# Kernel tuning notes

Measured on AMD Instinct MI355X. Metric: run time of the kernel, lower is better.

Reference implementation:

```python
import jax, jax.numpy as jnp
import numpy as np

N_NODES = 50000
N_EDGES = 1600000
N_GRAPHS = 1000


def setup_inputs() -> dict:
    key = jax.random.key(0)
    ks = jax.random.split(key, 16)
    s = 0.1
    return {
        "x": jax.random.normal(ks[0], (N_NODES, 7), jnp.float32),
        "edge_attr": jax.random.normal(ks[1], (N_EDGES, 4), jnp.float32),
        "edge_index": jax.random.randint(ks[2], (2, N_EDGES), 0, N_NODES),
        "batch": jnp.sort(jax.random.randint(ks[3], (N_NODES,), 0, N_GRAPHS)),
        "We1": jax.random.normal(ks[4], (4, 7), jnp.float32) * s,
        "be1": jnp.zeros((7,), jnp.float32),
        "W1a": jax.random.normal(ks[5], (7, 64), jnp.float32) * s,
        "b1a": jnp.zeros((64,), jnp.float32),
        "W1b": jax.random.normal(ks[6], (64, 64), jnp.float32) * s,
        "b1b": jnp.zeros((64,), jnp.float32),
        "We2": jax.random.normal(ks[7], (4, 64), jnp.float32) * s,
        "be2": jnp.zeros((64,), jnp.float32),
        "W2a": jax.random.normal(ks[8], (64, 64), jnp.float32) * s,
        "b2a": jnp.zeros((64,), jnp.float32),
        "W2b": jax.random.normal(ks[9], (64, 64), jnp.float32) * s,
        "b2b": jnp.zeros((64,), jnp.float32),
        "Wfc": jax.random.normal(ks[10], (64, 12), jnp.float32) * s,
        "bfc": jnp.zeros((12,), jnp.float32),
    }


def _gine_conv(h, edge_attr, src, dst, We, be, Wa, ba, Wb, bb, n_nodes):
    # GINEConv (eps=0): out = nn(h + sum_j relu(h[src] + lin(edge_attr)))
    e = edge_attr @ We + be                      # [E, d]
    msg = jax.nn.relu(h[src] + e)                # [E, d] gather + add + relu
    aggr = jax.ops.segment_sum(msg, dst, num_segments=n_nodes)  # scatter-sum
    z = h + aggr
    return jax.nn.relu(z @ Wa + ba) @ Wb + bb


def reference(x, edge_attr, edge_index, batch,
              We1, be1, W1a, b1a, W1b, b1b,
              We2, be2, W2a, b2a, W2b, b2b,
              Wfc, bfc):
    src, dst = edge_index[0], edge_index[1]
    n = x.shape[0]
    h = jax.nn.relu(_gine_conv(x, edge_attr, src, dst, We1, be1, W1a, b1a, W1b, b1b, n))
    h = jax.nn.relu(_gine_conv(h, edge_attr, src, dst, We2, be2, W2a, b2a, W2b, b2b, n))
    # global mean pool over batch index
    sums = jax.ops.segment_sum(h, batch, num_segments=N_GRAPHS)          # [G, 64]
    cnt = jax.ops.segment_sum(jnp.ones((n,), h.dtype), batch, num_segments=N_GRAPHS)
    pooled = sums / jnp.maximum(cnt, 1.0)[:, None]
    return pooled @ Wfc + bfc                                            # [G, 12]
```

## Files before the change

### kernel.cpp

```cpp
#include <hip/hip_runtime.h>

typedef unsigned char uchar;
typedef unsigned short ushort;
typedef unsigned int uint;

constexpr int NN = 50000;
constexpr int NE = 1600000;
constexpr int NG = 1000;
constexpr int NB2 = 196;
constexpr int TILE = 4096;
constexpr int NTILE = (NE + TILE - 1) / TILE;
constexpr int SPAN_CAP = 9216;
constexpr int MSTRIDE = 72;

constexpr int OFF_BCNT  = 0;
constexpr int OFF_SUMS  = 256;
constexpr int OFF_CNT   = 64256;
constexpr int ZERO_UNITS= 65280;
constexpr int OFF_BBASE = 65280;
constexpr int OFF_BCUR  = 65536;
constexpr int OFF_OFFS  = 65792;
constexpr int OFF_P0    = 116224;
constexpr int OFF_P1    = 1716224;
constexpr int OFF_P2    = 3316224;
constexpr int OFF_Z1    = 4916224;
constexpr int OFF_H1    = 5316224;
constexpr int OFF_Z     = 6916224;

typedef __attribute__((ext_vector_type(8))) short short8;
typedef __attribute__((ext_vector_type(4))) float float4v;

__device__ __forceinline__ uint f2bf(float f) {
    uint u = __float_as_uint(f);
    return (u + 0x7fffu + ((u >> 16) & 1u)) >> 16;
}
__device__ __forceinline__ float bf2f_lo(uint p) { return __uint_as_float(p << 16); }
__device__ __forceinline__ float bf2f_hi(uint p) { return __uint_as_float(p & 0xffff0000u); }

__global__ __launch_bounds__(256) void bhist_kernel(const int* __restrict__ eidx,
                                                    int* __restrict__ bcnt) {
    __shared__ int lh[NB2];
    for (int i = threadIdx.x; i < NB2; i += 256) lh[i] = 0;
    __syncthreads();
    int tid = blockIdx.x * 256 + threadIdx.x;
    int stride = gridDim.x * 256;
    for (int e = tid; e < NE; e += stride) atomicAdd(&lh[eidx[NE + e] >> 8], 1);
    __syncthreads();
    for (int i = threadIdx.x; i < NB2; i += 256) if (lh[i]) atomicAdd(&bcnt[i], lh[i]);
}

__global__ __launch_bounds__(256) void bscan_kernel(const int* __restrict__ bcnt,
                                                    int* __restrict__ bbase,
                                                    int* __restrict__ bcur) {
    __shared__ int s[256];
    int t = threadIdx.x;
    int v = (t < NB2) ? bcnt[t] : 0;
    s[t] = v; __syncthreads();
    for (int o = 1; o < 256; o <<= 1) {
        int u = (t >= o) ? s[t - o] : 0;
        __syncthreads();
        s[t] += u;
        __syncthreads();
    }
    bbase[t] = s[t] - v;
    bcur[t] = s[t] - v;
}

__global__ __launch_bounds__(256) void bin_kernel(const int* __restrict__ eidx,
                                                  const float4* __restrict__ ea,
                                                  int* __restrict__ bcur,
                                                  uint* __restrict__ p0,
                                                  uint* __restrict__ p1,
                                                  uint* __restrict__ p2) {
    __shared__ uint s0[TILE], s1[TILE], s2[TILE];
    __shared__ int hcnt[NB2], hoff[NB2 + 1], hcur[NB2], gbase[NB2];
    const int t = threadIdx.x;
    const int e0 = blockIdx.x * TILE;
    const int cnt = (NE - e0 < TILE) ? (NE - e0) : TILE;
    for (int i = t; i < NB2; i += 256) hcnt[i] = 0;
    __syncthreads();
    int dsts[16];
    #pragma unroll
    for (int k = 0; k < 16; ++k) {
        int i = t + k * 256;
        int d = (i < cnt) ? eidx[NE + e0 + i] : -1;
        dsts[k] = d;
        if (d >= 0) atomicAdd(&hcnt[d >> 8], 1);
    }
    __syncthreads();
    if (t == 0) {
        int a = 0;
        for (int b = 0; b < NB2; ++b) { hoff[b] = a; a += hcnt[b]; }
        hoff[NB2] = a;
    }
    __syncthreads();
    if (t < NB2) { hcur[t] = hoff[t]; gbase[t] = atomicAdd(&bcur[t], hcnt[t]); }
    __syncthreads();
    #pragma unroll
    for (int k = 0; k < 16; ++k) {
        int d = dsts[k];
        if (d < 0) continue;
        int i = t + k * 256;
        int e = e0 + i;
        int src = eidx[e];
        float4 a = ea[e];
        int lp = atomicAdd(&hcur[d >> 8], 1);
        s0[lp] = (uint)src | ((uint)(d & 255) << 16);
        s1[lp] = f2bf(a.x) | (f2bf(a.y) << 16);
        s2[lp] = f2bf(a.z) | (f2bf(a.w) << 16);
    }
    __syncthreads();
    for (int i = t; i < cnt; i += 256) {
        int lo = 0, hi = NB2 - 1;
        while (lo < hi) { int mid = (lo + hi + 1) >> 1; if (hoff[mid] <= i) lo = mid; else hi = mid - 1; }
        int gp = gbase[lo] + (i - hoff[lo]);
        p0[gp] = s0[i]; p1[gp] = s1[i]; p2[gp] = s2[i];
    }
}

__global__ __launch_bounds__(256) void build_kernel(const int* __restrict__ bbase,
                                                    const int* __restrict__ bcnt,
                                                    int* __restrict__ offs,
                                                    uint* __restrict__ p0,
                                                    uint* __restrict__ p1,
                                                    uint* __restrict__ p2) {
    __shared__ uint s0[SPAN_CAP], s1[SPAN_CAP], s2[SPAN_CAP];
    __shared__ int ldeg[256], lcur[256], sscan[256];
    const int t = threadIdx.x;
    const int b = blockIdx.x;
    const int nlo = b << 8;
    const int base = bbase[b];
    int span = bcnt[b];
    if (span > SPAN_CAP) span = SPAN_CAP;
    ldeg[t] = 0;
    __syncthreads();
    for (int i = t; i < span; i += 256)
        atomicAdd(&ldeg[(p0[base + i] >> 16) & 0xFFu], 1);
    __syncthreads();
    int v = ldeg[t];
    sscan[t] = v; __syncthreads();
    for (int o = 1; o < 256; o <<= 1) {
        int u = (t >= o) ? sscan[t - o] : 0;
        __syncthreads();
        sscan[t] += u;
        __syncthreads();
    }
    int exc = sscan[t] - v;
    lcur[t] = exc;
    int gi = nlo + t;
    if (gi < NN) offs[gi] = base + exc;
    else if (gi < 50176) offs[gi] = NE;
    __syncthreads();
    for (int i = t; i < span; i += 256) {
        uint r0 = p0[base + i], r1 = p1[base + i], r2 = p2[base + i];
        int pos = atomicAdd(&lcur[(r0 >> 16) & 0xFFu], 1);
        s0[pos] = r0; s1[pos] = r1; s2[pos] = r2;
    }
    __syncthreads();
    for (int i = t; i < span; i += 256) {
        p0[base + i] = s0[i]; p1[base + i] = s1[i]; p2[base + i] = s2[i];
    }
}

__global__ __launch_bounds__(256) void aggr1_kernel(
    const float* __restrict__ x,
    const uint* __restrict__ p0, const uint* __restrict__ p1, const uint* __restrict__ p2,
    const int* __restrict__ offs,
    const float* __restrict__ We1, const float* __restrict__ be1,
    float* __restrict__ z1)
{
    __shared__ float sWe[32];
    __shared__ float sbe[8];
    int tid = threadIdx.x;
    if (tid < 32) { int k = tid >> 3, dd = tid & 7; sWe[tid] = (dd < 7) ? We1[k * 7 + dd] : 0.f; }
    if (tid < 8)  sbe[tid] = (tid < 7) ? be1[tid] : 0.f;
    __syncthreads();

    const int w = tid >> 6, lane = tid & 63;
    const int jg = lane >> 3, d = lane & 7;

    for (int n = blockIdx.x * 4 + w; n < NN; n += gridDim.x * 4) {
        const int off = offs[n];
        const int deg = offs[n + 1] - off;
        float acc = 0.f;
        for (int j0 = 0; j0 < deg; j0 += 16) {
            int ja = j0 + jg;
            int jb = j0 + 8 + jg;
            int ia = off + ((ja < deg) ? ja : 0);
            int ib = off + ((jb < deg) ? jb : 0);
            uint r0a = p0[ia], r1a = p1[ia], r2a = p2[ia];
            uint r0b = p0[ib], r1b = p1[ib], r2b = p2[ib];
            float xa = (d < 7) ? x[(size_t)(r0a & 0xFFFFu) * 7 + d] : 0.f;
            float xb = (d < 7) ? x[(size_t)(r0b & 0xFFFFu) * 7 + d] : 0.f;
            float va = sbe[d] + bf2f_lo(r1a) * sWe[d] + bf2f_hi(r1a) * sWe[8 + d]
                     + bf2f_lo(r2a) * sWe[16 + d] + bf2f_hi(r2a) * sWe[24 + d] + xa;
            float vb = sbe[d] + bf2f_lo(r1b) * sWe[d] + bf2f_hi(r1b) * sWe[8 + d]
                     + bf2f_lo(r2b) * sWe[16 + d] + bf2f_hi(r2b) * sWe[24 + d] + xb;
            va = (d < 7 && ja < deg) ? fmaxf(va, 0.f) : 0.f;
            vb = (d < 7 && jb < deg) ? fmaxf(vb, 0.f) : 0.f;
            acc += va + vb;
        }
        acc += __shfl_xor(acc, 8);
        acc += __shfl_xor(acc, 16);
        acc += __shfl_xor(acc, 32);
        if (jg == 0)
            z1[(size_t)n * 8 + d] = (d < 7) ? (x[(size_t)n * 7 + d] + acc) : 0.f;
    }
}

__global__ __launch_bounds__(256) void node1_kernel(
    const float* __restrict__ z1,
    const float* __restrict__ W1a, const float* __restrict__ b1a,
    const float* __restrict__ W1b, const float* __restrict__ b1b,
    uint* __restrict__ h1u)
{
    __shared__ __align__(16) ushort sT[64 * MSTRIDE];
    __shared__ __align__(16) ushort sO[64 * 64];
    const int t = threadIdx.x;
    const int w = t >> 6, lane = t & 63;
    const int qm = lane & 15, quad = lane >> 4;
    const int n0 = blockIdx.x * 64;
    const int node = n0 + w * 16 + qm;

    short8 wa1n[4];
    #pragma unroll
    for (int nt = 0; nt < 4; ++nt) {
        short8 v = (short8)0;
        if (quad == 0) {
            #pragma unroll
            for (int j = 0; j < 7; ++j)
                v[j] = (short)f2bf(W1a[j * 64 + nt * 16 + qm]);
        }
        wa1n[nt] = v;
    }
    short8 wb1[2][4];
    #pragma unroll
    for (int s = 0; s < 2; ++s)
        #pragma unroll
        for (int nt = 0; nt < 4; ++nt) {
            short8 v;
            #pragma unroll
            for (int j = 0; j < 8; ++j)
                v[j] = (short)f2bf(W1b[(s * 32 + quad * 8 + j) * 64 + nt * 16 + qm]);
            wb1[s][nt] = v;
        }
    float ba[4], bb[4];
    #pragma unroll
    for (int nt = 0; nt < 4; ++nt) { ba[nt] = b1a[nt * 16 + qm]; bb[nt] = b1b[nt * 16 + qm]; }

    short8 af1 = (short8)0;
    if (quad == 0 && node < NN) {
        const float4 za = *(const float4*)(z1 + (size_t)node * 8);
        const float4 zbv = *(const float4*)(z1 + (size_t)node * 8 + 4);
        af1[0] = (short)f2bf(za.x); af1[1] = (short)f2bf(za.y);
        af1[2] = (short)f2bf(za.z); af1[3] = (short)f2bf(za.w);
        af1[4] = (short)f2bf(zbv.x); af1[5] = (short)f2bf(zbv.y);
        af1[6] = (short)f2bf(zbv.z); af1[7] = (short)f2bf(zbv.w);
    }
    float4v acc[4];
    #pragma unroll
    for (int nt = 0; nt < 4; ++nt) {
        acc[nt] = (float4v){0.f, 0.f, 0.f, 0.f};
        acc[nt] = __builtin_amdgcn_mfma_f32_16x16x32_bf16(af1, wa1n[nt], acc[nt], 0, 0, 0);
    }
    #pragma unroll
    for (int nt = 0; nt < 4; ++nt)
        #pragma unroll
        for (int r = 0; r < 4; ++r)
            sT[(w * 16 + quad * 4 + r) * MSTRIDE + nt * 16 + qm] =
                (ushort)f2bf(fmaxf(acc[nt][r] + ba[nt], 0.f));
    __syncthreads();

    #pragma unroll
    for (int nt = 0; nt < 4; ++nt) acc[nt] = (float4v){0.f, 0.f, 0.f, 0.f};
    #pragma unroll
    for (int s = 0; s < 2; ++s) {
        short8 af = *(const short8*)&sT[(w * 16 + qm) * MSTRIDE + s * 32 + quad * 8];
        #pragma unroll
        for (int nt = 0; nt < 4; ++nt)
            acc[nt] = __builtin_amdgcn_mfma_f32_16x16x32_bf16(af, wb1[s][nt], acc[nt], 0, 0, 0);
    }
    #pragma unroll
    for (int nt = 0; nt < 4; ++nt)
        #pragma unroll
        for (int r = 0; r < 4; ++r)
            sO[(w * 16 + quad * 4 + r) * 64 + nt * 16 + qm] =
                (ushort)f2bf(fmaxf(acc[nt][r] + bb[nt], 0.f));
    __syncthreads();
    for (int i = t; i < 64 * 32; i += 256) {
        int nd = i >> 5;
        if (n0 + nd < NN) h1u[(size_t)(n0 + nd) * 32 + (i & 31)] = ((const uint*)sO)[i];
    }
}

__global__ __launch_bounds__(256) void aggr2_kernel(
    const uint* __restrict__ h1u,
    const uint* __restrict__ p0, const uint* __restrict__ p1, const uint* __restrict__ p2,
    const int* __restrict__ offs,
    const float* __restrict__ We2, const float* __restrict__ be2,
    uint* __restrict__ zb)
{
    __shared__ float sWe[256];
    __shared__ float sbe[64];
    int tid = threadIdx.x;
    sWe[tid] = We2[tid];
    if (tid < 64) sbe[tid] = be2[tid];
    __syncthreads();
    const int w = tid >> 6, lane = tid & 63;
    const int l = lane & 31;
    const int half8 = (lane >> 5) << 3;
    const int n = blockIdx.x * 4 + w;
    const int off = offs[n];
    const int deg = offs[n + 1] - off;
    const float w0x = sWe[2 * l],       w0y = sWe[2 * l + 1];
    const float w1x = sWe[64 + 2 * l],  w1y = sWe[64 + 2 * l + 1];
    const float w2x = sWe[128 + 2 * l], w2y = sWe[128 + 2 * l + 1];
    const float w3x = sWe[192 + 2 * l], w3y = sWe[192 + 2 * l + 1];
    const float bbx = sbe[2 * l],       bby = sbe[2 * l + 1];

    float accx = 0.f, accy = 0.f;
    for (int jb = 0; jb < deg; jb += 16) {
        int m = deg - jb;
        int ll = (lane < 16) ? ((lane < m) ? lane : 0) : 0;
        int idx = off + jb + ll;
        int sx = (int)(p0[idx] & 0xFFFFu);
        uint e01 = p1[idx];
        uint e23 = p2[idx];
        uint g[8];
        #pragma unroll
        for (int k = 0; k < 8; ++k) {
            int mk = k + half8;
            int sk = __shfl(sx, (mk < m) ? mk : 0);
            g[k] = h1u[(size_t)sk * 32 + l];
        }
        #pragma unroll
        for (int k = 0; k < 8; ++k) {
            int mk = k + half8;
            int sl = (mk < m) ? mk : 0;
            uint py = (uint)__shfl((int)e01, sl);
            uint pz = (uint)__shfl((int)e23, sl);
            float e0 = bf2f_lo(py), e1 = bf2f_hi(py);
            float e2 = bf2f_lo(pz), e3 = bf2f_hi(pz);
            float bx = bbx + e0 * w0x + e1 * w1x + e2 * w2x + e3 * w3x;
            float by = bby + e0 * w0y + e1 * w1y + e2 * w2y + e3 * w3y;
            float tx = fmaxf(bf2f_lo(g[k]) + bx, 0.f);
            float ty = fmaxf(bf2f_hi(g[k]) + by, 0.f);
            if (mk < m) { accx += tx; accy += ty; }
        }
    }
    accx += __shfl_xor(accx, 32);
    accy += __shfl_xor(accy, 32);
    if (lane < 32) {
        uint sw = h1u[(size_t)n * 32 + l];
        float zx = bf2f_lo(sw) + accx;
        float zy = bf2f_hi(sw) + accy;
        zb[(size_t)n * 32 + l] = f2bf(zx) | (f2bf(zy) << 16);
    }
}

__global__ __launch_bounds__(256) void mlp2_kernel(
    const uint* __restrict__ zb,
    const float* __restrict__ W2a, const float* __restrict__ b2a,
    const float* __restrict__ W2b, const float* __restrict__ b2b,
    const int* __restrict__ batch,
    float* __restrict__ sums, float* __restrict__ cnt)
{
    __shared__ __align__(16) ushort sT[64 * MSTRIDE];
    __shared__ float sH[64 * 64];
    __shared__ int sB[64];
    __shared__ float pbuf[4][64];
    __shared__ int pcnt[4];
    const int t = threadIdx.x;
    const int w = t >> 6, lane = t & 63;
    const int qm = lane & 15, quad = lane >> 4;
    const int n0 = blockIdx.x * 64;
    const int node = n0 + w * 16 + qm;
    const int nv = (NN - n0 < 64) ? (NN - n0) : 64;

    if (t < 64) sB[t] = (n0 + t < NN) ? batch[n0 + t] : -2;

    short8 wa[2][4], wb[2][4];
    #pragma unroll
    for (int s = 0; s < 2; ++s)
        #pragma unroll
        for (int nt = 0; nt < 4; ++nt) {
            short8 va, vb;
            #pragma unroll
            for (int j = 0; j < 8; ++j) {
                int k = s * 32 + quad * 8 + j, n = nt * 16 + qm;
                va[j] = (short)f2bf(W2a[k * 64 + n]);
                vb[j] = (short)f2bf(W2b[k * 64 + n]);
            }
            wa[s][nt] = va; wb[s][nt] = vb;
        }
    float ba[4], bb[4];
    #pragma unroll
    for (int nt = 0; nt < 4; ++nt) { ba[nt] = b2a[nt * 16 + qm]; bb[nt] = b2b[nt * 16 + qm]; }

    float4v acc[4];
    #pragma unroll
    for (int nt = 0; nt < 4; ++nt) acc[nt] = (float4v){0.f, 0.f, 0.f, 0.f};
    #pragma unroll
    for (int s = 0; s < 2; ++s) {
        uint4 zw = (node < NN) ? *(const uint4*)&zb[(size_t)node * 32 + s * 16 + quad * 4]
                               : make_uint4(0, 0, 0, 0);
        short8 af;
        *(uint4*)&af = zw;
        #pragma unroll
        for (int nt = 0; nt < 4; ++nt)
            acc[nt] = __builtin_amdgcn_mfma_f32_16x16x32_bf16(af, wa[s][nt], acc[nt], 0, 0, 0);
    }
    #pragma unroll
    for (int nt = 0; nt < 4; ++nt)
        #pragma unroll
        for (int r = 0; r < 4; ++r)
            sT[(w * 16 + quad * 4 + r) * MSTRIDE + nt * 16 + qm] =
                (ushort)f2bf(fmaxf(acc[nt][r] + ba[nt], 0.f));
    __syncthreads();

    #pragma unroll
    for (int nt = 0; nt < 4; ++nt) acc[nt] = (float4v){0.f, 0.f, 0.f, 0.f};
    #pragma unroll
    for (int s = 0; s < 2; ++s) {
        short8 af = *(const short8*)&sT[(w * 16 + qm) * MSTRIDE + s * 32 + quad * 8];
        #pragma unroll
        for (int nt = 0; nt < 4; ++nt)
            acc[nt] = __builtin_amdgcn_mfma_f32_16x16x32_bf16(af, wb[s][nt], acc[nt], 0, 0, 0);
    }
    #pragma unroll
    for (int nt = 0; nt < 4; ++nt)
        #pragma unroll
        for (int r = 0; r < 4; ++r)
            sH[(w * 16 + quad * 4 + r) * 64 + nt * 16 + qm] = fmaxf(acc[nt][r] + bb[nt], 0.f);
    __syncthreads();

    const int glo = sB[0];
    const int ghi = sB[nv - 1];
    const int c = t >> 6, d = t & 63;
    for (int g = glo; g <= ghi; ++g) {
        float p = 0.f;
        int lc = 0;
        #pragma unroll 4
        for (int i = 0; i < 16; ++i) {
            int nd = c * 16 + i;
            if (sB[nd] == g) { p += sH[nd * 64 + d]; ++lc; }
        }
        pbuf[c][d] = p;
        if (d == 0) pcnt[c] = lc;
        __syncthreads();
        int tc = pcnt[0] + pcnt[1] + pcnt[2] + pcnt[3];
        if (tc > 0) {
            if (c == 0) {
                float tot = pbuf[0][d] + pbuf[1][d] + pbuf[2][d] + pbuf[3][d];
                atomicAdd(&sums[(size_t)g * 64 + d], tot);
            }
            if (t == 0) atomicAdd(&cnt[g], (float)tc);
        }
        __syncthreads();
    }
}

__global__ __launch_bounds__(256) void fc_kernel(
    const float* __restrict__ sums, const float* __restrict__ cnt,
    const float* __restrict__ Wfc, const float* __restrict__ bfc,
    float* __restrict__ out)
{
    int gid = blockIdx.x * blockDim.x + threadIdx.x;
    if (gid >= NG * 12) return;
    int g = gid / 12, jj = gid - g * 12;
    float inv = 1.f / fmaxf(cnt[g], 1.f);
    float acc = bfc[jj];
    #pragma unroll 8
    for (int k = 0; k < 64; ++k) acc += sums[(size_t)g * 64 + k] * inv * Wfc[k * 12 + jj];
    out[gid] = acc;
}

extern "C" void kernel_launch(void* const* d_in, const int* in_sizes, int n_in,
                              void* d_out, int out_size, void* d_ws, size_t ws_size,
                              hipStream_t stream)
{
    (void)in_sizes; (void)n_in; (void)out_size; (void)ws_size;
    const float*  x    = (const float*)d_in[0];
    const float4* ea   = (const float4*)d_in[1];
    const int*    eidx = (const int*)d_in[2];
    const int*    batch= (const int*)d_in[3];
    const float*  We1  = (const float*)d_in[4];
    const float*  be1  = (const float*)d_in[5];
    const float*  W1a  = (const float*)d_in[6];
    const float*  b1a  = (const float*)d_in[7];
    const float*  W1b  = (const float*)d_in[8];
    const float*  b1b  = (const float*)d_in[9];
    const float*  We2  = (const float*)d_in[10];
    const float*  be2  = (const float*)d_in[11];
    const float*  W2a  = (const float*)d_in[12];
    const float*  b2a  = (const float*)d_in[13];
    const float*  W2b  = (const float*)d_in[14];
    const float*  b2b  = (const float*)d_in[15];
    const float*  Wfc  = (const float*)d_in[16];
    const float*  bfc  = (const float*)d_in[17];
    float* out = (float*)d_out;
    float* ws  = (float*)d_ws;

    int*   bcnt  = (int*)(ws + OFF_BCNT);
    float* sums  = ws + OFF_SUMS;
    float* cnt   = ws + OFF_CNT;
    int*   bbase = (int*)(ws + OFF_BBASE);
    int*   bcur  = (int*)(ws + OFF_BCUR);
    int*   offs  = (int*)(ws + OFF_OFFS);
    uint*  p0    = (uint*)(ws + OFF_P0);
    uint*  p1    = (uint*)(ws + OFF_P1);
    uint*  p2    = (uint*)(ws + OFF_P2);
    float* z1    = ws + OFF_Z1;
    uint*  h1u   = (uint*)(ws + OFF_H1);
    uint*  zb    = (uint*)(ws + OFF_Z);

    hipMemsetAsync(d_ws, 0, (size_t)ZERO_UNITS * 4, stream);

    bhist_kernel<<<256, 256, 0, stream>>>(eidx, bcnt);
    bscan_kernel<<<1, 256, 0, stream>>>(bcnt, bbase, bcur);
    bin_kernel  <<<NTILE, 256, 0, stream>>>(eidx, ea, bcur, p0, p1, p2);
    build_kernel<<<NB2, 256, 0, stream>>>(bbase, bcnt, offs, p0, p1, p2);
    aggr1_kernel<<<2500, 256, 0, stream>>>(x, p0, p1, p2, offs, We1, be1, z1);
    node1_kernel<<<(NN + 63) / 64, 256, 0, stream>>>(z1, W1a, b1a, W1b, b1b, h1u);
    aggr2_kernel<<<12500, 256, 0, stream>>>(h1u, p0, p1, p2, offs, We2, be2, zb);
    mlp2_kernel <<<(NN + 63) / 64, 256, 0, stream>>>(zb, W2a, b2a, W2b, b2b, batch, sums, cnt);
    fc_kernel   <<<(NG * 12 + 255) / 256, 256, 0, stream>>>(sums, cnt, Wfc, bfc, out);
}
```

Baseline: 292.8 us.

## Remap aggr2 to one feature per lane with readlane edge broadcast

```diff
diff --git a/kernel.cpp b/kernel.cpp
--- a/kernel.cpp
+++ b/kernel.cpp
@@ -300,62 +300,49 @@
     const float* __restrict__ We2, const float* __restrict__ be2,
     uint* __restrict__ zb)
 {
-    __shared__ float sWe[256];
-    __shared__ float sbe[64];
-    int tid = threadIdx.x;
-    sWe[tid] = We2[tid];
-    if (tid < 64) sbe[tid] = be2[tid];
-    __syncthreads();
+    const int tid = threadIdx.x;
     const int w = tid >> 6, lane = tid & 63;
-    const int l = lane & 31;
-    const int half8 = (lane >> 5) << 3;
     const int n = blockIdx.x * 4 + w;
     const int off = offs[n];
     const int deg = offs[n + 1] - off;
-    const float w0x = sWe[2 * l],       w0y = sWe[2 * l + 1];
-    const float w1x = sWe[64 + 2 * l],  w1y = sWe[64 + 2 * l + 1];
-    const float w2x = sWe[128 + 2 * l], w2y = sWe[128 + 2 * l + 1];
-    const float w3x = sWe[192 + 2 * l], w3y = sWe[192 + 2 * l + 1];
-    const float bbx = sbe[2 * l],       bby = sbe[2 * l + 1];
-
-    float accx = 0.f, accy = 0.f;
-    for (int jb = 0; jb < deg; jb += 16) {
-        int m = deg - jb;
-        int ll = (lane < 16) ? ((lane < m) ? lane : 0) : 0;
-        int idx = off + jb + ll;
-        int sx = (int)(p0[idx] & 0xFFFFu);
-        uint e01 = p1[idx];
-        uint e23 = p2[idx];
-        uint g[8];
-        #pragma unroll
-        for (int k = 0; k < 8; ++k) {
-            int mk = k + half8;
-            int sk = __shfl(sx, (mk < m) ? mk : 0);
-            g[k] = h1u[(size_t)sk * 32 + l];
-        }
-        #pragma unroll
-        for (int k = 0; k < 8; ++k) {
-            int mk = k + half8;
-            int sl = (mk < m) ? mk : 0;
-            uint py = (uint)__shfl((int)e01, sl);
-            uint pz = (uint)__shfl((int)e23, sl);
-            float e0 = bf2f_lo(py), e1 = bf2f_hi(py);
-            float e2 = bf2f_lo(pz), e3 = bf2f_hi(pz);
-            float bx = bbx + e0 * w0x + e1 * w1x + e2 * w2x + e3 * w3x;
-            float by = bby + e0 * w0y + e1 * w1y + e2 * w2y + e3 * w3y;
-            float tx = fmaxf(bf2f_lo(g[k]) + bx, 0.f);
-            float ty = fmaxf(bf2f_hi(g[k]) + by, 0.f);
-            if (mk < m) { accx += tx; accy += ty; }
-        }
-    }
-    accx += __shfl_xor(accx, 32);
-    accy += __shfl_xor(accy, 32);
-    if (lane < 32) {
-        uint sw = h1u[(size_t)n * 32 + l];
-        float zx = bf2f_lo(sw) + accx;
-        float zy = bf2f_hi(sw) + accy;
-        zb[(size_t)n * 32 + l] = f2bf(zx) | (f2bf(zy) << 16);
-    }
+
+    const float w0 = We2[lane], w1 = We2[64 + lane], w2 = We2[128 + lane], w3 = We2[192 + lane];
+    const float bbv = be2[lane];
+
+    const ushort* hp = (const ushort*)h1u;
+    float acc = 0.f;
+
+    const int nb = deg & ~15;
+    for (int jb = 0; jb < nb; jb += 16) {
+        const int idx = off + jb + (lane & 15);
+        uint a0 = p0[idx];
+        uint a1 = p1[idx];
+        uint a2 = p2[idx];
+        #pragma unroll
+        for (int k = 0; k < 16; ++k) {
+            uint sk  = (uint)__builtin_amdgcn_readlane((int)a0, k) & 0xFFFFu;
+            uint e01 = (uint)__builtin_amdgcn_readlane((int)a1, k);
+            uint e23 = (uint)__builtin_amdgcn_readlane((int)a2, k);
+            float e0 = bf2f_lo(e01), e1 = bf2f_hi(e01);
+            float e2 = bf2f_lo(e23), e3 = bf2f_hi(e23);
+            float g = __uint_as_float((uint)hp[(size_t)sk * 64 + lane] << 16);
+            float b = bbv + e0 * w0 + e1 * w1 + e2 * w2 + e3 * w3;
+            acc += fmaxf(g + b, 0.f);
+        }
+    }
+    for (int j = nb; j < deg; ++j) {
+        uint r0 = p0[off + j];
+        uint r1 = p1[off + j];
+        uint r2 = p2[off + j];
+        uint sk = r0 & 0xFFFFu;
+        float g = __uint_as_float((uint)hp[(size_t)sk * 64 + lane] << 16);
+        float b = bbv + bf2f_lo(r1) * w0 + bf2f_hi(r1) * w1
+                + bf2f_lo(r2) * w2 + bf2f_hi(r2) * w3;
+        acc += fmaxf(g + b, 0.f);
+    }
+
+    float selfh = __uint_as_float((uint)hp[(size_t)n * 64 + lane] << 16);
+    ((ushort*)zb)[(size_t)n * 64 + lane] = (ushort)f2bf(selfh + acc);
 }
 
 __global__ __launch_bounds__(256) void mlp2_kernel(
```

Measured after the change: 314.6 us. +7.4%, slower.

## Fuse layer-1 edge aggregation into CSR build kernel using LDS atomics

Applied to the files above, without the earlier changes.

```diff
diff --git a/kernel.cpp b/kernel.cpp
--- a/kernel.cpp
+++ b/kernel.cpp
@@ -23,7 +23,7 @@
 constexpr int OFF_P0    = 116224;
 constexpr int OFF_P1    = 1716224;
 constexpr int OFF_P2    = 3316224;
-constexpr int OFF_Z1    = 4916224;
+constexpr int OFF_A1    = 4916224;
 constexpr int OFF_H1    = 5316224;
 constexpr int OFF_Z     = 6916224;
 
@@ -120,12 +120,19 @@
 
 __global__ __launch_bounds__(256) void build_kernel(const int* __restrict__ bbase,
                                                     const int* __restrict__ bcnt,
+                                                    const float* __restrict__ x,
+                                                    const float* __restrict__ We1,
+                                                    const float* __restrict__ be1,
                                                     int* __restrict__ offs,
                                                     uint* __restrict__ p0,
                                                     uint* __restrict__ p1,
-                                                    uint* __restrict__ p2) {
+                                                    uint* __restrict__ p2,
+                                                    float* __restrict__ aggr1) {
     __shared__ uint s0[SPAN_CAP], s1[SPAN_CAP], s2[SPAN_CAP];
     __shared__ int ldeg[256], lcur[256], sscan[256];
+    __shared__ float laggr[256][8];
+    __shared__ float sWe[32];
+    __shared__ float sbe[8];
     const int t = threadIdx.x;
     const int b = blockIdx.x;
     const int nlo = b << 8;
@@ -133,6 +140,10 @@
     int span = bcnt[b];
     if (span > SPAN_CAP) span = SPAN_CAP;
     ldeg[t] = 0;
+    if (t < 32) { int k = t >> 3, dd = t & 7; sWe[t] = (dd < 7) ? We1[k * 7 + dd] : 0.f; }
+    if (t < 8)  sbe[t] = (t < 7) ? be1[t] : 0.f;
+    #pragma unroll
+    for (int d = 0; d < 8; ++d) laggr[t][d] = 0.f;
     __syncthreads();
     for (int i = t; i < span; i += 256)
         atomicAdd(&ldeg[(p0[base + i] >> 16) & 0xFFu], 1);
@@ -158,58 +169,31 @@
     }
     __syncthreads();
     for (int i = t; i < span; i += 256) {
-        p0[base + i] = s0[i]; p1[base + i] = s1[i]; p2[base + i] = s2[i];
-    }
-}
-
-__global__ __launch_bounds__(256) void aggr1_kernel(
-    const float* __restrict__ x,
-    const uint* __restrict__ p0, const uint* __restrict__ p1, const uint* __restrict__ p2,
-    const int* __restrict__ offs,
-    const float* __restrict__ We1, const float* __restrict__ be1,
-    float* __restrict__ z1)
-{
-    __shared__ float sWe[32];
-    __shared__ float sbe[8];
-    int tid = threadIdx.x;
-    if (tid < 32) { int k = tid >> 3, dd = tid & 7; sWe[tid] = (dd < 7) ? We1[k * 7 + dd] : 0.f; }
-    if (tid < 8)  sbe[tid] = (tid < 7) ? be1[tid] : 0.f;
-    __syncthreads();
-
-    const int w = tid >> 6, lane = tid & 63;
-    const int jg = lane >> 3, d = lane & 7;
-
-    for (int n = blockIdx.x * 4 + w; n < NN; n += gridDim.x * 4) {
-        const int off = offs[n];
-        const int deg = offs[n + 1] - off;
-        float acc = 0.f;
-        for (int j0 = 0; j0 < deg; j0 += 16) {
-            int ja = j0 + jg;
-            int jb = j0 + 8 + jg;
-            int ia = off + ((ja < deg) ? ja : 0);
-            int ib = off + ((jb < deg) ? jb : 0);
-            uint r0a = p0[ia], r1a = p1[ia], r2a = p2[ia];
-            uint r0b = p0[ib], r1b = p1[ib], r2b = p2[ib];
-            float xa = (d < 7) ? x[(size_t)(r0a & 0xFFFFu) * 7 + d] : 0.f;
-            float xb = (d < 7) ? x[(size_t)(r0b & 0xFFFFu) * 7 + d] : 0.f;
-            float va = sbe[d] + bf2f_lo(r1a) * sWe[d] + bf2f_hi(r1a) * sWe[8 + d]
-                     + bf2f_lo(r2a) * sWe[16 + d] + bf2f_hi(r2a) * sWe[24 + d] + xa;
-            float vb = sbe[d] + bf2f_lo(r1b) * sWe[d] + bf2f_hi(r1b) * sWe[8 + d]
-                     + bf2f_lo(r2b) * sWe[16 + d] + bf2f_hi(r2b) * sWe[24 + d] + xb;
-            va = (d < 7 && ja < deg) ? fmaxf(va, 0.f) : 0.f;
-            vb = (d < 7 && jb < deg) ? fmaxf(vb, 0.f) : 0.f;
-            acc += va + vb;
-        }
-        acc += __shfl_xor(acc, 8);
-        acc += __shfl_xor(acc, 16);
-        acc += __shfl_xor(acc, 32);
-        if (jg == 0)
-            z1[(size_t)n * 8 + d] = (d < 7) ? (x[(size_t)n * 7 + d] + acc) : 0.f;
+        uint r0 = s0[i], r1 = s1[i], r2 = s2[i];
+        p0[base + i] = r0; p1[base + i] = r1; p2[base + i] = r2;
+        int src = (int)(r0 & 0xFFFFu);
+        int dl  = (int)((r0 >> 16) & 0xFFu);
+        float e0 = bf2f_lo(r1), e1 = bf2f_hi(r1);
+        float e2 = bf2f_lo(r2), e3 = bf2f_hi(r2);
+        const float* xs = x + (size_t)src * 7;
+        #pragma unroll
+        for (int d = 0; d < 7; ++d) {
+            float m = sbe[d] + e0 * sWe[d] + e1 * sWe[8 + d]
+                    + e2 * sWe[16 + d] + e3 * sWe[24 + d] + xs[d];
+            atomicAdd(&laggr[dl][d], fmaxf(m, 0.f));
+        }
+    }
+    __syncthreads();
+    if (nlo + t < NN) {
+        float4 a0 = make_float4(laggr[t][0], laggr[t][1], laggr[t][2], laggr[t][3]);
+        float4 a1 = make_float4(laggr[t][4], laggr[t][5], laggr[t][6], 0.f);
+        *(float4*)(aggr1 + (size_t)(nlo + t) * 8)     = a0;
+        *(float4*)(aggr1 + (size_t)(nlo + t) * 8 + 4) = a1;
     }
 }
 
 __global__ __launch_bounds__(256) void node1_kernel(
-    const float* __restrict__ z1,
+    const float* __restrict__ x, const float* __restrict__ aggr1,
     const float* __restrict__ W1a, const float* __restrict__ b1a,
     const float* __restrict__ W1b, const float* __restrict__ b1b,
     uint* __restrict__ h1u)
@@ -250,12 +234,13 @@
 
     short8 af1 = (short8)0;
     if (quad == 0 && node < NN) {
-        const float4 za = *(const float4*)(z1 + (size_t)node * 8);
-        const float4 zbv = *(const float4*)(z1 + (size_t)node * 8 + 4);
-        af1[0] = (short)f2bf(za.x); af1[1] = (short)f2bf(za.y);
-        af1[2] = (short)f2bf(za.z); af1[3] = (short)f2bf(za.w);
-        af1[4] = (short)f2bf(zbv.x); af1[5] = (short)f2bf(zbv.y);
-        af1[6] = (short)f2bf(zbv.z); af1[7] = (short)f2bf(zbv.w);
+        const float* xs = x + (size_t)node * 7;
+        const float4 a0 = *(const float4*)(aggr1 + (size_t)node * 8);
+        const float4 a1 = *(const float4*)(aggr1 + (size_t)node * 8 + 4);
+        af1[0] = (short)f2bf(xs[0] + a0.x); af1[1] = (short)f2bf(xs[1] + a0.y);
+        af1[2] = (short)f2bf(xs[2] + a0.z); af1[3] = (short)f2bf(xs[3] + a0.w);
+        af1[4] = (short)f2bf(xs[4] + a1.x); af1[5] = (short)f2bf(xs[5] + a1.y);
+        af1[6] = (short)f2bf(xs[6] + a1.z); af1[7] = 0;
     }
     float4v acc[4];
     #pragma unroll
@@ -510,7 +495,7 @@
     uint*  p0    = (uint*)(ws + OFF_P0);
     uint*  p1    = (uint*)(ws + OFF_P1);
     uint*  p2    = (uint*)(ws + OFF_P2);
-    float* z1    = ws + OFF_Z1;
+    float* aggr1 = ws + OFF_A1;
     uint*  h1u   = (uint*)(ws + OFF_H1);
     uint*  zb    = (uint*)(ws + OFF_Z);
 
@@ -519,9 +504,8 @@
     bhist_kernel<<<256, 256, 0, stream>>>(eidx, bcnt);
     bscan_kernel<<<1, 256, 0, stream>>>(bcnt, bbase, bcur);
     bin_kernel  <<<NTILE, 256, 0, stream>>>(eidx, ea, bcur, p0, p1, p2);
-    build_kernel<<<NB2, 256, 0, stream>>>(bbase, bcnt, offs, p0, p1, p2);
-    aggr1_kernel<<<2500, 256, 0, stream>>>(x, p0, p1, p2, offs, We1, be1, z1);
-    node1_kernel<<<(NN + 63) / 64, 256, 0, stream>>>(z1, W1a, b1a, W1b, b1b, h1u);
+    build_kernel<<<NB2, 256, 0, stream>>>(bbase, bcnt, x, We1, be1, offs, p0, p1, p2, aggr1);
+    node1_kernel<<<(NN + 63) / 64, 256, 0, stream>>>(x, aggr1, W1a, b1a, W1b, b1b, h1u);
     aggr2_kernel<<<12500, 256, 0, stream>>>(h1u, p0, p1, p2, offs, We2, be2, zb);
     mlp2_kernel <<<(NN + 63) / 64, 256, 0, stream>>>(zb, W2a, b2a, W2b, b2b, batch, sums, cnt);
     fc_kernel   <<<(NG * 12 + 255) / 256, 256, 0, stream>>>(sums, cnt, Wfc, bfc, out);
```

New measurement: 363.8 us. 24.2% more time.
